# Optimization experiments

Hardware: AMD Instinct MI355X
Metric: run time of the kernel (lower is better)

## Reference

```python
import jax, jax.numpy as jnp
import numpy as np

B, S, D = 32, 2048, 1024
TEMP = 9.0  # RelaxedBernoulli temperature (torch.tensor([9]))


def setup_inputs() -> dict:
    key = jax.random.key(0)
    ks = jax.random.split(key, 12)
    sd = 1.0 / np.sqrt(D)
    sd2 = 1.0 / np.sqrt(2 * D)
    return {
        "h_t": jax.random.normal(ks[0], (B, D), jnp.float32),
        "h_s": jax.random.normal(ks[1], (B, S, D), jnp.float32),
        "auxi_hs": jax.random.normal(ks[2], (B, S, D), jnp.float32),
        "noise_u": jax.random.uniform(ks[3], (B, S, 1), jnp.float32),
        # linear_map: Linear(2*dim, 1) with bias
        "Wmap": jax.random.normal(ks[4], (2 * D,), jnp.float32) * sd2,
        "bmap": jax.random.normal(ks[5], (), jnp.float32) * sd2,
        # mlp_h: Linear(dim, dim) + Tanh + Linear(dim, 1)
        "W1": jax.random.normal(ks[6], (D, D), jnp.float32) * sd,
        "b1": jax.random.normal(ks[7], (D,), jnp.float32) * sd,
        "W2": jax.random.normal(ks[8], (D,), jnp.float32) * sd,
        "b2": jax.random.normal(ks[9], (), jnp.float32) * sd,
        # linear_out: Linear(2*dim, dim, bias=False) (attn_type='dot')
        "Wout": jax.random.normal(ks[10], (D, 2 * D), jnp.float32) * sd2,
    }


def reference(h_t, h_s, auxi_hs, noise_u, Wmap, bmap, W1, b1, W2, b2, Wout):
    # h_t: (B, D) one-step query; h_s, auxi_hs: (B, S, D)
    d = h_s.shape[-1]
    # linear_map(concat(auxi_hs, H_t)) without materializing the (B,S,2D) concat
    Wm_a, Wm_t = Wmap[:d], Wmap[d:]
    logits_p = jnp.einsum('bsd,d->bs', auxi_hs, Wm_a) + (h_t @ Wm_t)[:, None] + bmap  # (B,S)
    logits_p = logits_p[..., None]  # (B,S,1); note logit(sigmoid(x)) == x
    # RelaxedBernoulli(temp=9, probs=sigmoid(logits_p)).sample() with explicit uniform noise
    eps = 1e-7
    u = jnp.clip(noise_u, eps, 1.0 - eps)
    logistic = jnp.log(u) - jnp.log1p(-u)  # (B,S,1)
    G = jax.nn.sigmoid((logits_p + logistic) / TEMP)  # (B,S,1)
    # mlp_h(h_s): Linear -> tanh -> Linear
    e = jnp.einsum('bsd,d->bs', jnp.tanh(jnp.einsum('bsd,ed->bse', h_s, W1) + b1), W2) + b2
    e = e[..., None]  # (B,S,1)
    # custom softmax: max over dim 0 (batch!), exp, gate
    v = jnp.max(e, axis=0, keepdims=True)  # (1,S,1)
    scores = jnp.exp(e - v) * G  # (B,S,1)
    align = scores[..., 0] / jnp.sum(scores[..., 0], axis=1, keepdims=True)  # (B,S)
    c = jnp.einsum('bs,bsd->bd', align, h_s)  # (B,D)
    attn_h = jnp.tanh(jnp.concatenate([c, h_t], axis=-1) @ Wout.T)  # (B,D)
    return attn_h, align
```

## Files before the change

### kernel.cpp

```cpp
#include <hip/hip_runtime.h>
#include <hip/hip_bf16.h>
#include <math.h>

#define B_ 32
#define S_ 2048
#define D_ 1024
#define TEMP_ 9.0f

typedef __attribute__((ext_vector_type(8))) short short8;
typedef __attribute__((ext_vector_type(4))) float f32x4;
typedef __attribute__((ext_vector_type(4))) unsigned short ushort4v;

__device__ __forceinline__ unsigned short f2b(float f) {
  union { float f; unsigned int u; } v; v.f = f;
  unsigned int r = v.u;
  r += 0x7fffu + ((r >> 16) & 1u);
  return (unsigned short)(r >> 16);
}
__device__ __forceinline__ float b2f(unsigned short b) {
  union { float f; unsigned int u; } v; v.u = ((unsigned int)b) << 16;
  return v.f;
}
__device__ __forceinline__ float tanh_fast(float x) {
  float ez = __expf(2.f * x);
  return 1.f - __fdividef(2.f, ez + 1.f);
}

#define GLOAD_LDS16(g, l) \
  __builtin_amdgcn_global_load_lds((const __attribute__((address_space(1))) void*)(g), \
                                   (__attribute__((address_space(3))) void*)(l), 16, 0, 0)

__global__ void k_conv(const float* __restrict__ src, unsigned short* __restrict__ dst, int n8) {
  int i = blockIdx.x * 256 + threadIdx.x;
  if (i >= n8) return;
  const float4* g = reinterpret_cast<const float4*>(src) + (size_t)i * 2;
  float4 x0 = g[0], x1 = g[1];
  uint4 w;
  w.x = f2b(x0.x) | ((unsigned)f2b(x0.y) << 16);
  w.y = f2b(x0.z) | ((unsigned)f2b(x0.w) << 16);
  w.z = f2b(x1.x) | ((unsigned)f2b(x1.y) << 16);
  w.w = f2b(x1.z) | ((unsigned)f2b(x1.w) << 16);
  reinterpret_cast<uint4*>(dst)[i] = w;
}

__global__ void k_pack_w1(const float* __restrict__ W1, unsigned short* __restrict__ w1t) {
  int c = blockIdx.x * 256 + threadIdx.x;
  int l  = c & 63;
  int kt = (c >> 6) & 31;
  int cg = c >> 11;
  int col = cg * 16 + (l & 15);
  int k0  = kt * 32 + (l >> 4) * 8;
  const float* src = W1 + (size_t)col * D_ + k0;
  float4 x0 = *reinterpret_cast<const float4*>(src);
  float4 x1 = *reinterpret_cast<const float4*>(src + 4);
  uint4 w;
  w.x = f2b(x0.x) | ((unsigned)f2b(x0.y) << 16);
  w.y = f2b(x0.z) | ((unsigned)f2b(x0.w) << 16);
  w.z = f2b(x1.x) | ((unsigned)f2b(x1.y) << 16);
  w.w = f2b(x1.z) | ((unsigned)f2b(x1.w) << 16);
  reinterpret_cast<uint4*>(w1t)[c] = w;
}

__global__ void k0_tdot(const float* __restrict__ h_t, const float* __restrict__ Wmap,
                        const float* __restrict__ bmap, float* __restrict__ tdot) {
  int b = blockIdx.x;
  int t = threadIdx.x;
  float p = 0.f;
  for (int k = t; k < D_; k += 256) p += h_t[b*D_ + k] * Wmap[D_ + k];
  __shared__ float red[256];
  red[t] = p; __syncthreads();
  for (int off = 128; off > 0; off >>= 1) { if (t < off) red[t] += red[t+off]; __syncthreads(); }
  if (t == 0) tdot[b] = red[0] + bmap[0];
}

__global__ void k1_gate(const float* __restrict__ aux, const float* __restrict__ Wmap,
                        const float* __restrict__ noise, const float* __restrict__ tdot,
                        float* __restrict__ Gout) {
  int w = (blockIdx.x * 256 + threadIdx.x) >> 6;
  int lane = threadIdx.x & 63;
  const float4* arow = reinterpret_cast<const float4*>(aux + (size_t)w * D_);
  const float4* wrow = reinterpret_cast<const float4*>(Wmap);
  float p = 0.f;
  for (int it = 0; it < 4; ++it) {
    float4 a = arow[it*64 + lane];
    float4 m = wrow[it*64 + lane];
    p += a.x*m.x + a.y*m.y + a.z*m.z + a.w*m.w;
  }
  for (int msk = 32; msk > 0; msk >>= 1) p += __shfl_xor(p, msk);
  if (lane == 0) {
    int b = w >> 11;
    float logits = p + tdot[b];
    float u = noise[w];
    u = fminf(fmaxf(u, 1e-7f), 1.f - 1e-7f);
    float logistic = logf(u) - log1pf(-u);
    float x = (logits + logistic) / TEMP_;
    Gout[w] = 1.f / (1.f + expf(-x));
  }
}

#define NT3 32

extern __shared__ unsigned short lds2[];

__global__ __launch_bounds__(256, 2) void k2_breg(
    const unsigned short* __restrict__ Ag, const unsigned short* __restrict__ w1t,
    const float* __restrict__ b1, const float* __restrict__ W2,
    float* __restrict__ e_buf) {
  int hw = blockIdx.x;
  int xcd = hw & 7;
  int sub = hw >> 3;
  int cc  = sub & 3;
  int rc  = xcd + 8 * (sub >> 2);
  int rowBase = rc * 128;
  int colBase = cc * 256;

  int t = threadIdx.x;
  int lane = t & 63;
  int wv = t >> 6;
  int kslot = lane >> 4;

  int aOff[8];
#pragma unroll
  for (int m = 0; m < 8; ++m) {
    int r = m * 16 + (lane & 15);
    aOff[m] = r * 64 + ((kslot ^ ((r >> 1) & 3)) << 4);
  }

  const unsigned short* gA[2];
  int dstA[2];
#pragma unroll
  for (int i = 0; i < 2; ++i) {
    int c = i * 256 + t;
    int r = c >> 2;
    int clog = (c & 3) ^ ((r >> 1) & 3);
    gA[i] = Ag + (size_t)(rowBase + r) * D_ + clog * 8;
    dstA[i] = c * 16;
  }

  const unsigned short* pB[4];
#pragma unroll
  for (int n = 0; n < 4; ++n) {
    int cg = (colBase >> 4) + wv * 4 + n;
    pB[n] = w1t + (size_t)cg * 16384 + lane * 8;
  }

  f32x4 acc[8][4] = {};
  short8 bfA[4], bfB[4];

#define STAGE(TT) do {                                                         \
    char* _ba = (char*)lds2 + ((TT) & 3) * 8192;                               \
    GLOAD_LDS16(gA[0] + (TT) * 32, _ba + dstA[0]);                             \
    GLOAD_LDS16(gA[1] + (TT) * 32, _ba + dstA[1]);                             \
  } while (0)

#define K2_TILE(T, VM, DO_B, DO_S, BFC, BFN) do {                              \
    asm volatile("s_waitcnt lgkmcnt(0)\n\ts_waitcnt vmcnt(" #VM ")" ::: "memory"); \
    __builtin_amdgcn_s_barrier();                                              \
    const char* _ab = (const char*)lds2 + ((T) & 3) * 8192;                    \
    short8 af[8];                                                              \
    _Pragma("unroll")                                                          \
    for (int m = 0; m < 8; ++m)                                                \
      af[m] = *reinterpret_cast<const short8*>(_ab + aOff[m]);                 \
    if (DO_B) {                                                                \
      _Pragma("unroll")                                                        \
      for (int n = 0; n < 4; ++n)                                              \
        BFN[n] = *reinterpret_cast<const short8*>(pB[n] + ((T) + 1) * 512);    \
    }                                                                          \
    if (DO_S) STAGE((T) + 3);                                                  \
    __builtin_amdgcn_s_setprio(1);                                             \
    _Pragma("unroll")                                                          \
    for (int m = 0; m < 8; ++m)                                                \
      _Pragma("unroll")                                                        \
      for (int n = 0; n < 4; ++n)                                              \
        acc[m][n] = __builtin_amdgcn_mfma_f32_16x16x32_bf16(af[m], BFC[n], acc[m][n], 0, 0, 0); \
    __builtin_amdgcn_s_setprio(0);                                             \
  } while (0)

  STAGE(0); STAGE(1); STAGE(2);
#pragma unroll
  for (int n = 0; n < 4; ++n)
    bfA[n] = *reinterpret_cast<const short8*>(pB[n]);

  K2_TILE(0, 0, true, true, bfA, bfB);
  K2_TILE(1, 2, true, true, bfB, bfA);
#pragma unroll
  for (int tt = 2; tt < 28; tt += 2) {
    K2_TILE(tt,     2, true, true, bfA, bfB);
    K2_TILE(tt + 1, 2, true, true, bfB, bfA);
  }
  K2_TILE(28, 2, true,  true,  bfA, bfB);
  K2_TILE(29, 2, true,  false, bfB, bfA);
  K2_TILE(30, 0, true,  false, bfA, bfB);
  K2_TILE(31, 0, false, false, bfB, bfA);
#undef K2_TILE
#undef STAGE

  float b1v[4], w2v[4];
#pragma unroll
  for (int n = 0; n < 4; ++n) {
    int col = colBase + wv * 64 + n * 16 + (lane & 15);
    b1v[n] = b1[col];
    w2v[n] = W2[col];
  }
#pragma unroll
  for (int m = 0; m < 8; ++m) {
#pragma unroll
    for (int j = 0; j < 4; ++j) {
      float s = 0.f;
#pragma unroll
      for (int n = 0; n < 4; ++n)
        s += tanh_fast(acc[m][n][j] + b1v[n]) * w2v[n];
      s += __shfl_xor(s, 1);
      s += __shfl_xor(s, 2);
      s += __shfl_xor(s, 4);
      s += __shfl_xor(s, 8);
      if ((lane & 15) == 0) {
        int row = rowBase + m * 16 + ((lane >> 4) << 2) + j;
        atomicAdd(&e_buf[row], s);
      }
    }
  }
}

#define BM 128
#define BN 128
#define BK 64
__global__ __launch_bounds__(256) void k2_egemm_f32(
    const float* __restrict__ h_s, const float* __restrict__ W1,
    const float* __restrict__ b1, const float* __restrict__ W2,
    float* __restrict__ e_buf) {
  __shared__ unsigned short As[BM * BK];
  __shared__ unsigned short Bs[BN * BK];
  int bid = blockIdx.x;
  int colBase = (bid & 7) * BN;
  int rowBase = (bid >> 3) * BM;
  int t = threadIdx.x;
  int lane = t & 63;
  int wave = t >> 6;
  int wr = wave >> 1, wc = wave & 1;
  f32x4 acc[4][4] = {};
  for (int k0 = 0; k0 < D_; k0 += BK) {
    __syncthreads();
    for (int i = 0; i < 4; ++i) {
      int flat = i*256 + t;
      int r = flat >> 3;
      int c8 = flat & 7;
      int byte = (r*128 + c8*16) ^ ((r & 7) << 4);
      {
        const float4* g = reinterpret_cast<const float4*>(h_s + (size_t)(rowBase + r)*D_ + k0 + c8*8);
        float4 x0 = g[0], x1 = g[1];
        uint4 w;
        w.x = f2b(x0.x) | ((unsigned)f2b(x0.y) << 16);
        w.y = f2b(x0.z) | ((unsigned)f2b(x0.w) << 16);
        w.z = f2b(x1.x) | ((unsigned)f2b(x1.y) << 16);
        w.w = f2b(x1.z) | ((unsigned)f2b(x1.w) << 16);
        *reinterpret_cast<uint4*>(reinterpret_cast<char*>(As) + byte) = w;
      }
      {
        const float4* g = reinterpret_cast<const float4*>(W1 + (size_t)(colBase + r)*D_ + k0 + c8*8);
        float4 x0 = g[0], x1 = g[1];
        uint4 w;
        w.x = f2b(x0.x) | ((unsigned)f2b(x0.y) << 16);
        w.y = f2b(x0.z) | ((unsigned)f2b(x0.w) << 16);
        w.z = f2b(x1.x) | ((unsigned)f2b(x1.y) << 16);
        w.w = f2b(x1.z) | ((unsigned)f2b(x1.w) << 16);
        *reinterpret_cast<uint4*>(reinterpret_cast<char*>(Bs) + byte) = w;
      }
    }
    __syncthreads();
    for (int kk = 0; kk < BK; kk += 32) {
      short8 af[4], bf[4];
      int kByte = kk*2 + ((lane >> 4) << 4);
      for (int m = 0; m < 4; ++m) {
        int r = wr*64 + m*16 + (lane & 15);
        int byte = (r*128 + kByte) ^ ((r & 7) << 4);
        af[m] = *reinterpret_cast<const short8*>(reinterpret_cast<const char*>(As) + byte);
      }
      for (int n = 0; n < 4; ++n) {
        int r = wc*64 + n*16 + (lane & 15);
        int byte = (r*128 + kByte) ^ ((r & 7) << 4);
        bf[n] = *reinterpret_cast<const short8*>(reinterpret_cast<const char*>(Bs) + byte);
      }
      for (int m = 0; m < 4; ++m)
        for (int n = 0; n < 4; ++n)
          acc[m][n] = __builtin_amdgcn_mfma_f32_16x16x32_bf16(af[m], bf[n], acc[m][n], 0, 0, 0);
    }
  }
  float b1v[4], w2v[4];
  for (int n = 0; n < 4; ++n) {
    int col = colBase + wc*64 + n*16 + (lane & 15);
    b1v[n] = b1[col];
    w2v[n] = W2[col];
  }
  for (int m = 0; m < 4; ++m) {
    for (int j = 0; j < 4; ++j) {
      float s = 0.f;
      for (int n = 0; n < 4; ++n)
        s += tanhf(acc[m][n][j] + b1v[n]) * w2v[n];
      s += __shfl_xor(s, 1);
      s += __shfl_xor(s, 2);
      s += __shfl_xor(s, 4);
      s += __shfl_xor(s, 8);
      if ((lane & 15) == 0) {
        int row = rowBase + wr*64 + m*16 + ((lane >> 4) << 2) + j;
        atomicAdd(&e_buf[row], s);
      }
    }
  }
}

__global__ void k3a_vmax(const float* __restrict__ e_buf, float* __restrict__ v) {
  int s = blockIdx.x * 256 + threadIdx.x;
  if (s >= S_) return;
  float m = -1e30f;
  for (int b = 0; b < B_; ++b) m = fmaxf(m, e_buf[b*S_ + s]);
  v[s] = m;
}

__global__ void k3b_align(const float* __restrict__ e_buf, const float* __restrict__ v,
                          float* __restrict__ galign) {
  int b = blockIdx.x;
  int t = threadIdx.x;
  __shared__ float sc[S_];
  __shared__ float red[256];
  float p = 0.f;
  for (int s = t; s < S_; s += 256) {
    float x = expf(e_buf[b*S_ + s] - v[s]) * galign[b*S_ + s];
    sc[s] = x;
    p += x;
  }
  red[t] = p; __syncthreads();
  for (int off = 128; off > 0; off >>= 1) { if (t < off) red[t] += red[t+off]; __syncthreads(); }
  float inv = 1.f / red[0];
  for (int s = t; s < S_; s += 256) galign[b*S_ + s] = sc[s] * inv;
}

__global__ void k4_ctx_bf16(const unsigned short* __restrict__ hsb, const float* __restrict__ align,
                            float* __restrict__ c) {
  int bid = blockIdx.x;
  int b = bid >> 6;
  int sBase = (bid & 63) * 32;
  int t = threadIdx.x;
  float4 accv = {0.f, 0.f, 0.f, 0.f};
  for (int si = 0; si < 32; ++si) {
    int s = sBase + si;
    float a = align[b*S_ + s];
    ushort4v hv = *reinterpret_cast<const ushort4v*>(hsb + (size_t)(b*S_ + s)*D_ + t*4);
    accv.x += a*b2f(hv.x); accv.y += a*b2f(hv.y); accv.z += a*b2f(hv.z); accv.w += a*b2f(hv.w);
  }
  atomicAdd(&c[b*D_ + t*4 + 0], accv.x);
  atomicAdd(&c[b*D_ + t*4 + 1], accv.y);
  atomicAdd(&c[b*D_ + t*4 + 2], accv.z);
  atomicAdd(&c[b*D_ + t*4 + 3], accv.w);
}

__global__ void k4_ctx_f32(const float* __restrict__ h_s, const float* __restrict__ align,
                           float* __restrict__ c) {
  int bid = blockIdx.x;
  int b = bid >> 6;
  int sBase = (bid & 63) * 32;
  int t = threadIdx.x;
  float4 accv = {0.f, 0.f, 0.f, 0.f};
  for (int si = 0; si < 32; ++si) {
    int s = sBase + si;
    float a = align[b*S_ + s];
    float4 hv = *reinterpret_cast<const float4*>(h_s + (size_t)(b*S_ + s)*D_ + t*4);
    accv.x += a*hv.x; accv.y += a*hv.y; accv.z += a*hv.z; accv.w += a*hv.w;
  }
  atomicAdd(&c[b*D_ + t*4 + 0], accv.x);
  atomicAdd(&c[b*D_ + t*4 + 1], accv.y);
  atomicAdd(&c[b*D_ + t*4 + 2], accv.z);
  atomicAdd(&c[b*D_ + t*4 + 3], accv.w);
}

__global__ void k5_out(const float* __restrict__ c, const float* __restrict__ h_t,
                       const float* __restrict__ Wout, float* __restrict__ out) {
  int W = (blockIdx.x * 256 + threadIdx.x) >> 6;
  int lane = threadIdx.x & 63;
  int b = W >> 10;
  int o = W & 1023;
  const float* wrow = Wout + (size_t)o * (2 * D_);
  float p = 0.f;
  for (int it = 0; it < 16; ++it) {
    int k = it*64 + lane;
    p += c[b*D_ + k] * wrow[k];
  }
  for (int it = 16; it < 32; ++it) {
    int k = it*64 + lane;
    p += h_t[b*D_ + (k - D_)] * wrow[k];
  }
  for (int m = 32; m > 0; m >>= 1) p += __shfl_xor(p, m);
  if (lane == 0) out[b*D_ + o] = tanhf(p);
}

extern "C" void kernel_launch(void* const* d_in, const int* in_sizes, int n_in,
                              void* d_out, int out_size, void* d_ws, size_t ws_size,
                              hipStream_t stream) {
  const float* h_t   = (const float*)d_in[0];
  const float* h_s   = (const float*)d_in[1];
  const float* aux   = (const float*)d_in[2];
  const float* noise = (const float*)d_in[3];
  const float* Wmap  = (const float*)d_in[4];
  const float* bmap  = (const float*)d_in[5];
  const float* W1    = (const float*)d_in[6];
  const float* b1    = (const float*)d_in[7];
  const float* W2    = (const float*)d_in[8];
  const float* Wout  = (const float*)d_in[10];

  float* out    = (float*)d_out;
  float* galign = out + B_*D_;

  const size_t HS_N   = (size_t)B_*S_*D_;
  const size_t W1_N   = (size_t)D_*D_;
  const size_t needed = HS_N*2 + W1_N*2 + (65536 + 32 + 2048 + 32768) * sizeof(float);

  if (ws_size >= needed) {
    unsigned short* hs_bf = (unsigned short*)d_ws;
    unsigned short* w1t   = hs_bf + HS_N;
    float* fws   = (float*)(w1t + W1_N);
    float* e_buf = fws;
    float* tdot  = fws + 65536;
    float* v     = fws + 65568;
    float* c     = fws + 67616;

    hipMemsetAsync(e_buf, 0, 65536 * sizeof(float), stream);
    hipMemsetAsync(c, 0, 32768 * sizeof(float), stream);

    hipFuncSetAttribute(reinterpret_cast<const void*>(k2_breg),
                        hipFuncAttributeMaxDynamicSharedMemorySize, 32768);

    k_conv<<<(int)(HS_N/8/256), 256, 0, stream>>>(h_s, hs_bf, (int)(HS_N/8));
    k_pack_w1<<<512, 256, 0, stream>>>(W1, w1t);
    k0_tdot<<<32, 256, 0, stream>>>(h_t, Wmap, bmap, tdot);
    k1_gate<<<16384, 256, 0, stream>>>(aux, Wmap, noise, tdot, galign);
    k2_breg<<<2048, 256, 32768, stream>>>(hs_bf, w1t, b1, W2, e_buf);
    k3a_vmax<<<8, 256, 0, stream>>>(e_buf, v);
    k3b_align<<<32, 256, 0, stream>>>(e_buf, v, galign);
    k4_ctx_bf16<<<2048, 256, 0, stream>>>(hs_bf, galign, c);
    k5_out<<<8192, 256, 0, stream>>>(c, h_t, Wout, out);
  } else {
    float* ws    = (float*)d_ws;
    float* e_buf = ws;
    float* tdot  = ws + 65536;
    float* v     = ws + 65568;
    float* c     = ws + 67616;

    hipMemsetAsync(e_buf, 0, 65536 * sizeof(float), stream);
    hipMemsetAsync(c, 0, 32768 * sizeof(float), stream);

    k0_tdot<<<32, 256, 0, stream>>>(h_t, Wmap, bmap, tdot);
    k1_gate<<<16384, 256, 0, stream>>>(aux, Wmap, noise, tdot, galign);
    k2_egemm_f32<<<4096, 256, 0, stream>>>(h_s, W1, b1, W2, e_buf);
    k3a_vmax<<<8, 256, 0, stream>>>(e_buf, v);
    k3b_align<<<32, 256, 0, stream>>>(e_buf, v, galign);
    k4_ctx_f32<<<2048, 256, 0, stream>>>(h_s, galign, c);
    k5_out<<<8192, 256, 0, stream>>>(c, h_t, Wout, out);
  }
}
```

Before: 353.3 us.

## Fuse gate computation into bf16 GEMM kernel as extra leading blocks

The separate k1_gate launch is merged into the GEMM kernel: the first 1024 blocks compute the RelaxedBernoulli gate from auxi_hs, and the remaining blocks run the unchanged bf16 MLP GEMM. Each gate wave now handles 16 rows with Wmap held in registers instead of one row per wave. This removes a kernel launch and lets the memory-bound gate pass run alongside the compute-bound GEMM. In exchange, the gate blocks are held to the GEMM's launch bounds and 32 KB dynamic LDS allocation, which may limit how many of them run at once.

```diff
diff --git a/kernel.cpp b/kernel.cpp
--- a/kernel.cpp
+++ b/kernel.cpp
@@ -98,25 +98,53 @@
   }
 }
 
-#define NT3 32
-
 extern __shared__ unsigned short lds2[];
 
-__global__ __launch_bounds__(256, 2) void k2_breg(
+__global__ __launch_bounds__(256, 2) void k2g(
     const unsigned short* __restrict__ Ag, const unsigned short* __restrict__ w1t,
     const float* __restrict__ b1, const float* __restrict__ W2,
-    float* __restrict__ e_buf) {
-  int hw = blockIdx.x;
+    float* __restrict__ e_buf,
+    const float* __restrict__ aux, const float* __restrict__ Wmap,
+    const float* __restrict__ noise, const float* __restrict__ tdot,
+    float* __restrict__ Gout) {
+  int bid = blockIdx.x;
+  int t = threadIdx.x;
+  int lane = t & 63;
+  int wv = t >> 6;
+
+  if (bid < 1024) {
+    const float4* wrow = reinterpret_cast<const float4*>(Wmap);
+    float4 m0 = wrow[lane], m1 = wrow[64 + lane], m2 = wrow[128 + lane], m3 = wrow[192 + lane];
+    int gw = (bid << 2) | wv;
+#pragma unroll 2
+    for (int i = 0; i < 16; ++i) {
+      int row = (gw << 4) | i;
+      const float4* arow = reinterpret_cast<const float4*>(aux + (size_t)row * D_);
+      float4 a0 = arow[lane], a1 = arow[64 + lane], a2 = arow[128 + lane], a3 = arow[192 + lane];
+      float p = a0.x*m0.x + a0.y*m0.y + a0.z*m0.z + a0.w*m0.w
+              + a1.x*m1.x + a1.y*m1.y + a1.z*m1.z + a1.w*m1.w
+              + a2.x*m2.x + a2.y*m2.y + a2.z*m2.z + a2.w*m2.w
+              + a3.x*m3.x + a3.y*m3.y + a3.z*m3.z + a3.w*m3.w;
+      for (int msk = 32; msk > 0; msk >>= 1) p += __shfl_xor(p, msk);
+      if (lane == 0) {
+        float logits = p + tdot[row >> 11];
+        float u = noise[row];
+        u = fminf(fmaxf(u, 1e-7f), 1.f - 1e-7f);
+        float logistic = logf(u) - log1pf(-u);
+        float x = (logits + logistic) / TEMP_;
+        Gout[row] = 1.f / (1.f + expf(-x));
+      }
+    }
+    return;
+  }
+
+  int hw = bid - 1024;
   int xcd = hw & 7;
   int sub = hw >> 3;
   int cc  = sub & 3;
   int rc  = xcd + 8 * (sub >> 2);
   int rowBase = rc * 128;
   int colBase = cc * 256;
-
-  int t = threadIdx.x;
-  int lane = t & 63;
-  int wv = t >> 6;
   int kslot = lane >> 4;
 
   int aOff[8];
@@ -426,14 +454,14 @@
     hipMemsetAsync(e_buf, 0, 65536 * sizeof(float), stream);
     hipMemsetAsync(c, 0, 32768 * sizeof(float), stream);
 
-    hipFuncSetAttribute(reinterpret_cast<const void*>(k2_breg),
+    hipFuncSetAttribute(reinterpret_cast<const void*>(k2g),
                         hipFuncAttributeMaxDynamicSharedMemorySize, 32768);
 
     k_conv<<<(int)(HS_N/8/256), 256, 0, stream>>>(h_s, hs_bf, (int)(HS_N/8));
     k_pack_w1<<<512, 256, 0, stream>>>(W1, w1t);
     k0_tdot<<<32, 256, 0, stream>>>(h_t, Wmap, bmap, tdot);
-    k1_gate<<<16384, 256, 0, stream>>>(aux, Wmap, noise, tdot, galign);
-    k2_breg<<<2048, 256, 32768, stream>>>(hs_bf, w1t, b1, W2, e_buf);
+    k2g<<<3072, 256, 32768, stream>>>(hs_bf, w1t, b1, W2, e_buf,
+                                      aux, Wmap, noise, tdot, galign);
     k3a_vmax<<<8, 256, 0, stream>>>(e_buf, v);
     k3b_align<<<32, 256, 0, stream>>>(e_buf, v, galign);
     k4_ctx_bf16<<<2048, 256, 0, stream>>>(hs_bf, galign, c);
```

New measurement: 355.7 us. About the same (+0.7%).

## Fuse gate computation into the MLP GEMM kernel to overlap aux streaming

Applied to the files above, without the earlier changes.

Removes the separate k1_gate launch and folds the per-row aux·Wmap dot product plus the relaxed-Bernoulli gate into the k2 GEMM main loop. Each wave loads one float4 of aux per K tile, interleaved with the MFMA work, so the memory-bound aux read overlaps with compute-bound matrix work. The vmcnt wait counts are raised to account for the extra outstanding global loads. The cost is more registers and more VMEM traffic inside the GEMM loop, which could hurt occupancy or the pipeline timing.

```diff
diff --git a/kernel.cpp b/kernel.cpp
--- a/kernel.cpp
+++ b/kernel.cpp
@@ -98,17 +98,18 @@
   }
 }
 
-#define NT3 32
-
 extern __shared__ unsigned short lds2[];
 
-__global__ __launch_bounds__(256, 2) void k2_breg(
+__global__ __launch_bounds__(256, 2) void k2gi(
     const unsigned short* __restrict__ Ag, const unsigned short* __restrict__ w1t,
     const float* __restrict__ b1, const float* __restrict__ W2,
-    float* __restrict__ e_buf) {
-  int hw = blockIdx.x;
-  int xcd = hw & 7;
-  int sub = hw >> 3;
+    float* __restrict__ e_buf,
+    const float* __restrict__ aux, const float* __restrict__ Wmap,
+    const float* __restrict__ noise, const float* __restrict__ tdot,
+    float* __restrict__ Gout) {
+  int bid = blockIdx.x;
+  int xcd = bid & 7;
+  int sub = bid >> 3;
   int cc  = sub & 3;
   int rc  = xcd + 8 * (sub >> 2);
   int rowBase = rc * 128;
@@ -143,6 +144,39 @@
     int cg = (colBase >> 4) + wv * 4 + n;
     pB[n] = w1t + (size_t)cg * 16384 + lane * 8;
   }
+
+  const float4* wrow = reinterpret_cast<const float4*>(Wmap);
+  float4 gm0 = wrow[lane], gm1 = wrow[64 + lane], gm2 = wrow[128 + lane], gm3 = wrow[192 + lane];
+  int rowG = (bid << 5) | (wv << 3);
+  const float* gAux = aux + ((size_t)rowG << 10) + (lane << 2);
+  float4 gbuf;
+  float gacc = 0.f;
+
+#define GATE_FIN(PR) do {                                                      \
+    float p = gacc;                                                            \
+    for (int msk = 32; msk > 0; msk >>= 1) p += __shfl_xor(p, msk);            \
+    if (lane == 0) {                                                           \
+      int row = rowG + ((PR) >> 2);                                            \
+      float logits = p + tdot[row >> 11];                                      \
+      float u = noise[row];                                                    \
+      u = fminf(fmaxf(u, 1e-7f), 1.f - 1e-7f);                                 \
+      float logistic = logf(u) - log1pf(-u);                                   \
+      float x = (logits + logistic) / TEMP_;                                   \
+      Gout[row] = 1.f / (1.f + expf(-x));                                      \
+    }                                                                          \
+    gacc = 0.f;                                                                \
+  } while (0)
+
+#define GATE_STEP(T) do {                                                      \
+    if ((T) >= 1) {                                                            \
+      int pr = (T) - 1;                                                        \
+      float4 mm = ((pr & 3) == 0) ? gm0 : ((pr & 3) == 1) ? gm1                \
+                : ((pr & 3) == 2) ? gm2 : gm3;                                 \
+      gacc += gbuf.x*mm.x + gbuf.y*mm.y + gbuf.z*mm.z + gbuf.w*mm.w;           \
+      if ((pr & 3) == 3) GATE_FIN(pr);                                         \
+    }                                                                          \
+    gbuf = *reinterpret_cast<const float4*>(gAux + (((T) >> 2) << 10) + (((T) & 3) << 8)); \
+  } while (0)
 
   f32x4 acc[8][4] = {};
   short8 bfA[4], bfB[4];
@@ -167,6 +201,7 @@
         BFN[n] = *reinterpret_cast<const short8*>(pB[n] + ((T) + 1) * 512);    \
     }                                                                          \
     if (DO_S) STAGE((T) + 3);                                                  \
+    GATE_STEP(T);                                                              \
     __builtin_amdgcn_s_setprio(1);                                             \
     _Pragma("unroll")                                                          \
     for (int m = 0; m < 8; ++m)                                                \
@@ -181,19 +216,24 @@
   for (int n = 0; n < 4; ++n)
     bfA[n] = *reinterpret_cast<const short8*>(pB[n]);
 
-  K2_TILE(0, 0, true, true, bfA, bfB);
-  K2_TILE(1, 2, true, true, bfB, bfA);
+  K2_TILE(0, 4, true, true, bfA, bfB);
+  K2_TILE(1, 8, true, true, bfB, bfA);
 #pragma unroll
   for (int tt = 2; tt < 28; tt += 2) {
-    K2_TILE(tt,     2, true, true, bfA, bfB);
-    K2_TILE(tt + 1, 2, true, true, bfB, bfA);
-  }
-  K2_TILE(28, 2, true,  true,  bfA, bfB);
-  K2_TILE(29, 2, true,  false, bfB, bfA);
-  K2_TILE(30, 0, true,  false, bfA, bfB);
-  K2_TILE(31, 0, false, false, bfB, bfA);
+    K2_TILE(tt,     8, true, true, bfA, bfB);
+    K2_TILE(tt + 1, 8, true, true, bfB, bfA);
+  }
+  K2_TILE(28, 8, true,  true,  bfA, bfB);
+  K2_TILE(29, 8, true,  false, bfB, bfA);
+  K2_TILE(30, 8, true,  false, bfA, bfB);
+  K2_TILE(31, 8, false, false, bfB, bfA);
 #undef K2_TILE
 #undef STAGE
+
+  gacc += gbuf.x*gm3.x + gbuf.y*gm3.y + gbuf.z*gm3.z + gbuf.w*gm3.w;
+  GATE_FIN(31);
+#undef GATE_STEP
+#undef GATE_FIN
 
   float b1v[4], w2v[4];
 #pragma unroll
@@ -426,14 +466,14 @@
     hipMemsetAsync(e_buf, 0, 65536 * sizeof(float), stream);
     hipMemsetAsync(c, 0, 32768 * sizeof(float), stream);
 
-    hipFuncSetAttribute(reinterpret_cast<const void*>(k2_breg),
+    hipFuncSetAttribute(reinterpret_cast<const void*>(k2gi),
                         hipFuncAttributeMaxDynamicSharedMemorySize, 32768);
 
     k_conv<<<(int)(HS_N/8/256), 256, 0, stream>>>(h_s, hs_bf, (int)(HS_N/8));
     k_pack_w1<<<512, 256, 0, stream>>>(W1, w1t);
     k0_tdot<<<32, 256, 0, stream>>>(h_t, Wmap, bmap, tdot);
-    k1_gate<<<16384, 256, 0, stream>>>(aux, Wmap, noise, tdot, galign);
-    k2_breg<<<2048, 256, 32768, stream>>>(hs_bf, w1t, b1, W2, e_buf);
+    k2gi<<<2048, 256, 32768, stream>>>(hs_bf, w1t, b1, W2, e_buf,
+                                       aux, Wmap, noise, tdot, galign);
     k3a_vmax<<<8, 256, 0, stream>>>(e_buf, v);
     k3b_align<<<32, 256, 0, stream>>>(e_buf, v, galign);
     k4_ctx_bf16<<<2048, 256, 0, stream>>>(hs_bf, galign, c);
```

After: 508.6 us. +43.9%, slower.
